# Optimization experiments

Hardware: AMD Instinct MI355X
Metric: run time of the kernel (lower is better)

Reference implementation:

```python
import jax, jax.numpy as jnp
import numpy as np

N, D, E = 100000, 64, 1250000


def setup_inputs() -> dict:
    key = jax.random.key(0)
    k0, k1, k2, k3, k4 = jax.random.split(key, 5)
    return {
        "old_g": jax.random.normal(k0, (N, D), dtype=jnp.float32),        # node DB features
        "W": jax.random.normal(k1, (D, D), dtype=jnp.float32) / np.sqrt(D).astype(np.float32),  # method params
        "edge_weight": jax.random.uniform(k2, (E, 1), dtype=jnp.float32), # per-edge method values
        "history_db": jnp.zeros((N, D), dtype=jnp.float32),               # db_layer.history_db
        "src": jax.random.randint(k3, (E,), 0, N, dtype=jnp.int32),       # gather pattern (sender)
        "dst": jax.random.randint(k4, (E,), 0, N, dtype=jnp.int32),       # scatter index (receiver)
    }


def reference(old_g, W, edge_weight, history_db, src, dst):
    # grab_db_to_method: transform node DB once, then irregular per-edge gather of rows
    h = old_g @ W                                   # [N, D]
    # calc_batch: per-edge method call on gathered sender/receiver features
    msg = jnp.tanh(h[src] + old_g[dst] * edge_weight)  # [E, D]
    # finish_step: scatter-add results back into node-indexed state arrays
    agg = jax.ops.segment_sum(msg, dst, num_segments=old_g.shape[0])  # [N, D]
    nodes_new = agg                   # nodes.at[idx].set(all_results)
    history_new = history_db + agg    # history_db.at[idx].add(all_results)
    return nodes_new, history_new
```

## Files before the change

### kernel.cpp

```cpp
#include <hip/hip_runtime.h>
#include <hip/hip_bf16.h>
#include <hip/hip_fp16.h>


#define D_FEAT 64
#define WQ_SCALE 32767.0f
#define WQ_INV   (1.0f / 32767.0f)
#define BSHIFT 9
#define BN     (1 << BSHIFT)
#define NBUCK_MAX 256
#define BCAP   8192
#define PA_BLOCKS 512
#define PA_CHUNK_MAX 2560

typedef int v4i __attribute__((ext_vector_type(4)));
typedef int v2i __attribute__((ext_vector_type(2)));

#define GR 128
#define GPAD 66

__global__ __launch_bounds__(256) void gemm64_tile_kernel(
    const float* __restrict__ g, const float* __restrict__ W,
    __half* __restrict__ h16, int N, int* __restrict__ bcur) {
    __shared__ float Wl[D_FEAT * D_FEAT];
    __shared__ float Gl[GR][GPAD];

    const int tid = threadIdx.x;

    if (blockIdx.x == 0) bcur[tid] = tid * BCAP;

    {
        const float4* w4 = reinterpret_cast<const float4*>(W);
        float4* wl4 = reinterpret_cast<float4*>(Wl);
        for (int i = tid; i < D_FEAT * D_FEAT / 4; i += 256) wl4[i] = w4[i];
    }

    const int row0  = blockIdx.x * GR;
    const int nrows = min(GR, N - row0);

    for (int i = tid; i < GR * 16; i += 256) {
        const int r  = i >> 4;
        const int c4 = i & 15;
        if (r < nrows) {
            float4 v = reinterpret_cast<const float4*>(
                           g + (size_t)(row0 + r) * D_FEAT)[c4];
            float* dp = &Gl[r][c4 * 4];
            reinterpret_cast<float2*>(dp)[0] = make_float2(v.x, v.y);
            reinterpret_cast<float2*>(dp)[1] = make_float2(v.z, v.w);
        }
    }
    __syncthreads();

    const int cg = tid & 7;
    const int rg = tid >> 3;
    const int c0 = cg * 8;
    const int r0 = rg * 4;

    float acc[4][8];
#pragma unroll
    for (int i = 0; i < 4; ++i)
#pragma unroll
        for (int j = 0; j < 8; ++j) acc[i][j] = 0.0f;

#pragma unroll 4
    for (int k = 0; k < D_FEAT; ++k) {
        const float4 wa = *reinterpret_cast<const float4*>(&Wl[k * D_FEAT + c0]);
        const float4 wb = *reinterpret_cast<const float4*>(&Wl[k * D_FEAT + c0 + 4]);
        float gv[4];
#pragma unroll
        for (int i = 0; i < 4; ++i) gv[i] = Gl[r0 + i][k];
#pragma unroll
        for (int i = 0; i < 4; ++i) {
            acc[i][0] = fmaf(gv[i], wa.x, acc[i][0]);
            acc[i][1] = fmaf(gv[i], wa.y, acc[i][1]);
            acc[i][2] = fmaf(gv[i], wa.z, acc[i][2]);
            acc[i][3] = fmaf(gv[i], wa.w, acc[i][3]);
            acc[i][4] = fmaf(gv[i], wb.x, acc[i][4]);
            acc[i][5] = fmaf(gv[i], wb.y, acc[i][5]);
            acc[i][6] = fmaf(gv[i], wb.z, acc[i][6]);
            acc[i][7] = fmaf(gv[i], wb.w, acc[i][7]);
        }
    }

#pragma unroll
    for (int i = 0; i < 4; ++i) {
        const int r = r0 + i;
        if (r < nrows) {
            __half2 hb[4];
#pragma unroll
            for (int j = 0; j < 4; ++j)
                hb[j] = __floats2half2_rn(acc[i][2 * j], acc[i][2 * j + 1]);
            *reinterpret_cast<uint4*>(h16 + (size_t)(row0 + r) * D_FEAT + c0) =
                *reinterpret_cast<uint4*>(hb);
        }
    }
}

__device__ __forceinline__ unsigned pack_edge(int s, float w) {
    int wq = __float2int_rn(w * WQ_SCALE);
    wq = min(wq, 32767);
    wq = max(wq, 0);
    return (unsigned)s | ((unsigned)wq << 17);
}

__global__ __launch_bounds__(256) void bucketA_kernel(
    const int* __restrict__ src, const int* __restrict__ dst,
    const float* __restrict__ ew, int* __restrict__ bcur,
    int2* __restrict__ staged, int E, int chunk, int nbuck) {
    __shared__ int2 stage[PA_CHUNK_MAX];
    __shared__ int cnt[NBUCK_MAX], startb[NBUCK_MAX], baseb[NBUCK_MAX],
                   cnt2[NBUCK_MAX], sc[NBUCK_MAX];
    const int tid = threadIdx.x;
    const int beg = blockIdx.x * chunk;
    const int end = min(beg + chunk, E);
    const int n = end - beg;
    if (n <= 0) return;

    if (tid < NBUCK_MAX) { cnt[tid] = 0; cnt2[tid] = 0; }
    __syncthreads();

    for (int i = tid; i < n; i += 256)
        atomicAdd(&cnt[dst[beg + i] >> BSHIFT], 1);
    __syncthreads();

    sc[tid] = (tid < nbuck) ? cnt[tid] : 0;
    __syncthreads();
    for (int off = 1; off < NBUCK_MAX; off <<= 1) {
        int x = (tid >= off) ? sc[tid - off] : 0;
        __syncthreads();
        sc[tid] += x;
        __syncthreads();
    }
    if (tid < nbuck) {
        startb[tid] = sc[tid] - cnt[tid];
        if (cnt[tid] > 0) baseb[tid] = atomicAdd(&bcur[tid], cnt[tid]);
    }
    __syncthreads();

    for (int i = tid; i < n; i += 256) {
        const int d = dst[beg + i];
        const int b = d >> BSHIFT;
        const unsigned pl = pack_edge(src[beg + i], ew[beg + i]);
        const int lp = atomicAdd(&cnt2[b], 1);
        stage[startb[b] + lp] = make_int2(d, (int)pl);
    }
    __syncthreads();

    for (int i = tid; i < n; i += 256) {
        const int2 en = stage[i];
        const int b = en.x >> BSHIFT;
        staged[baseb[b] + (i - startb[b])] = en;
    }
}

__global__ __launch_bounds__(256) void bucketB_kernel(
    const int2* __restrict__ staged, const int* __restrict__ bcur,
    int2* __restrict__ nodeinfo, unsigned* __restrict__ srcw,
    int N, int nbuck) {
    __shared__ int cnt[BN];
    __shared__ int cur[BN];
    __shared__ int sc[256];
    const int b = blockIdx.x;
    const int tid = threadIdx.x;
    const int node0 = b << BSHIFT;
    const int beg = b * BCAP;
    const int end = bcur[b];

    cnt[tid] = 0;
    cnt[tid + 256] = 0;
    __syncthreads();

    for (int i = beg + tid; i < end; i += 256) {
        const int2 en = staged[i];
        atomicAdd(&cnt[en.x - node0], 1);
    }
    __syncthreads();

    const int c0 = cnt[2 * tid];
    const int c1 = cnt[2 * tid + 1];
    const int s = c0 + c1;
    sc[tid] = s;
    __syncthreads();
    for (int off = 1; off < 256; off <<= 1) {
        int x = (tid >= off) ? sc[tid - off] : 0;
        __syncthreads();
        sc[tid] += x;
        __syncthreads();
    }
    const int excl = sc[tid] - s + beg;
    {
        const int n0 = node0 + 2 * tid;
        if (n0 < N) {
            nodeinfo[n0] = make_int2(excl, c0);
            cur[2 * tid] = excl;
        }
        if (n0 + 1 < N) {
            nodeinfo[n0 + 1] = make_int2(excl + c0, c1);
            cur[2 * tid + 1] = excl + c0;
        }
    }
    __syncthreads();

    for (int i = beg + tid; i < end; i += 256) {
        const int2 en = staged[i];
        const int pos = atomicAdd(&cur[en.x - node0], 1);
        srcw[pos] = (unsigned)en.y;
    }
}

__device__ __forceinline__ float fast_tanh(float x) {
    float e = __builtin_amdgcn_exp2f(2.885390082f * x);
    float r = __builtin_amdgcn_rcpf(1.0f + e);
    return fmaf(-2.0f, r, 1.0f);
}

__global__ void node_kernel(const __half* __restrict__ h16,
                            const float* __restrict__ g,
                            const float* __restrict__ hist,
                            const int2* __restrict__ nodeinfo,
                            const unsigned* __restrict__ srcw,
                            float* __restrict__ out_nodes,
                            float* __restrict__ out_hist, int N) {
    const int lane = threadIdx.x & 63;
    const int wid  = threadIdx.x >> 6;
    const int wpb  = blockDim.x >> 6;
    const int slot = lane >> 4;
    const int fg   = lane & 15;

    for (int n = blockIdx.x * wpb + wid; n < N; n += gridDim.x * wpb) {
        const int2 info = nodeinfo[n];
        const int beg = info.x;
        const int end = beg + info.y;
        const float4 gd = *reinterpret_cast<const float4*>(
            g + (size_t)n * D_FEAT + fg * 4);
        const float4 hv4 = *reinterpret_cast<const float4*>(
            hist + (size_t)n * D_FEAT + fg * 4);

        float4 acc = make_float4(0.0f, 0.0f, 0.0f, 0.0f);

        for (int base = beg; base < end; base += 64) {
            const int chunk = min(64, end - base);
            const unsigned my_sw = srcw[base + min(lane, chunk - 1)];

            for (int g0 = 0; g0 < chunk; g0 += 8) {
                const int ia = g0 + slot;
                const int ib = ia + 4;
                const unsigned pa = (unsigned)__shfl((int)my_sw, ia, 64);
                const unsigned pb = (unsigned)__shfl((int)my_sw, ib, 64);
                const int   sa = pa & 0x1FFFF;
                const float wa = (float)(pa >> 17) * WQ_INV;
                const int   sb = pb & 0x1FFFF;
                const float wb = (float)(pb >> 17) * WQ_INV;
                const bool va = ia < chunk;
                const bool vb = ib < chunk;
                const uint2 hva = *reinterpret_cast<const uint2*>(
                    h16 + (size_t)sa * D_FEAT + fg * 4);
                const uint2 hvb = *reinterpret_cast<const uint2*>(
                    h16 + (size_t)sb * D_FEAT + fg * 4);

                const float2 a0 = __half22float2(
                    *reinterpret_cast<const __half2*>(&hva.x));
                const float2 a1 = __half22float2(
                    *reinterpret_cast<const __half2*>(&hva.y));
                const float ma = va ? 1.0f : 0.0f;
                acc.x = fmaf(ma, fast_tanh(fmaf(gd.x, wa, a0.x)), acc.x);
                acc.y = fmaf(ma, fast_tanh(fmaf(gd.y, wa, a0.y)), acc.y);
                acc.z = fmaf(ma, fast_tanh(fmaf(gd.z, wa, a1.x)), acc.z);
                acc.w = fmaf(ma, fast_tanh(fmaf(gd.w, wa, a1.y)), acc.w);

                const float2 b0 = __half22float2(
                    *reinterpret_cast<const __half2*>(&hvb.x));
                const float2 b1 = __half22float2(
                    *reinterpret_cast<const __half2*>(&hvb.y));
                const float mb = vb ? 1.0f : 0.0f;
                acc.x = fmaf(mb, fast_tanh(fmaf(gd.x, wb, b0.x)), acc.x);
                acc.y = fmaf(mb, fast_tanh(fmaf(gd.y, wb, b0.y)), acc.y);
                acc.z = fmaf(mb, fast_tanh(fmaf(gd.z, wb, b1.x)), acc.z);
                acc.w = fmaf(mb, fast_tanh(fmaf(gd.w, wb, b1.y)), acc.w);
            }
        }

        acc.x += __shfl_xor(acc.x, 16, 64);
        acc.y += __shfl_xor(acc.y, 16, 64);
        acc.z += __shfl_xor(acc.z, 16, 64);
        acc.w += __shfl_xor(acc.w, 16, 64);
        acc.x += __shfl_xor(acc.x, 32, 64);
        acc.y += __shfl_xor(acc.y, 32, 64);
        acc.z += __shfl_xor(acc.z, 32, 64);
        acc.w += __shfl_xor(acc.w, 32, 64);

        if (lane < 16) {
            reinterpret_cast<float4*>(out_nodes + (size_t)n * D_FEAT)[fg] = acc;
            float4 o;
            o.x = acc.x + hv4.x;
            o.y = acc.y + hv4.y;
            o.z = acc.z + hv4.z;
            o.w = acc.w + hv4.w;
            reinterpret_cast<float4*>(out_hist + (size_t)n * D_FEAT)[fg] = o;
        }
    }
}

extern "C" void kernel_launch(void* const* d_in, const int* in_sizes, int n_in,
                              void* d_out, int out_size, void* d_ws, size_t ws_size,
                              hipStream_t stream) {
    const float* old_g = (const float*)d_in[0];
    const float* W     = (const float*)d_in[1];
    const float* ew    = (const float*)d_in[2];
    const float* hist  = (const float*)d_in[3];
    const int*   src   = (const int*)d_in[4];
    const int*   dst   = (const int*)d_in[5];

    const int N  = in_sizes[0] / D_FEAT;
    const int E  = in_sizes[4];
    const int ND = N * D_FEAT;
    const int nbuck = (N + BN - 1) >> BSHIFT;

    float* out_nodes = (float*)d_out;
    float* out_hist  = (float*)d_out + ND;

    char* ws = (char*)d_ws;
    __half* h16     = (__half*)ws;               ws += (size_t)ND * 2;
    int*  bcur      = (int*)ws;                  ws += 256 * 4;
    int2* nodeinfo  = (int2*)ws;                 ws += (size_t)(N + 2) * 8;
    unsigned* srcw  = (unsigned*)ws;             ws += (size_t)nbuck * BCAP * 4;
    int2* staged    = (int2*)ws;

    {
        int grid = (N + GR - 1) / GR;
        gemm64_tile_kernel<<<grid, 256, 0, stream>>>(old_g, W, h16, N, bcur);
    }

    {
        const int chunk = (E + PA_BLOCKS - 1) / PA_BLOCKS;
        bucketA_kernel<<<PA_BLOCKS, 256, 0, stream>>>(src, dst, ew, bcur,
                                                      staged, E, chunk, nbuck);
    }

    bucketB_kernel<<<nbuck, 256, 0, stream>>>(staged, bcur, nodeinfo,
                                              srcw, N, nbuck);

    {
        const int block = 256, wpb = block / 64;
        int grid = (N + wpb - 1) / wpb;
        if (grid > 8192) grid = 8192;
        node_kernel<<<grid, block, 0, stream>>>(h16, old_g, hist, nodeinfo,
                                                srcw, out_nodes, out_hist, N);
    }
}
```

Before: 103.7 us.

## Merge GEMM and bucket-partition kernels into one launch with block-range dispatch

The node-feature GEMM and the first edge-bucketing pass now run as a single horizontally fused kernel. Low block indices do the GEMM tile and the rest do bucket partitioning, sharing one shared-memory buffer. Bucket cursors are now zero-initialised by a memset and treated as relative offsets, because the GEMM kernel no longer initialises them before bucketing starts. The aim is to remove one kernel launch boundary and let the two independent phases overlap, at the cost of an extra memset and a larger shared-memory footprint per block.

```diff
diff --git a/kernel.cpp b/kernel.cpp
--- a/kernel.cpp
+++ b/kernel.cpp
@@ -13,88 +13,12 @@
 #define PA_BLOCKS 512
 #define PA_CHUNK_MAX 2560
 
+#define GR 128
+#define GPAD 66
+#define SMEM_BYTES 50176
+
 typedef int v4i __attribute__((ext_vector_type(4)));
 typedef int v2i __attribute__((ext_vector_type(2)));
-
-#define GR 128
-#define GPAD 66
-
-__global__ __launch_bounds__(256) void gemm64_tile_kernel(
-    const float* __restrict__ g, const float* __restrict__ W,
-    __half* __restrict__ h16, int N, int* __restrict__ bcur) {
-    __shared__ float Wl[D_FEAT * D_FEAT];
-    __shared__ float Gl[GR][GPAD];
-
-    const int tid = threadIdx.x;
-
-    if (blockIdx.x == 0) bcur[tid] = tid * BCAP;
-
-    {
-        const float4* w4 = reinterpret_cast<const float4*>(W);
-        float4* wl4 = reinterpret_cast<float4*>(Wl);
-        for (int i = tid; i < D_FEAT * D_FEAT / 4; i += 256) wl4[i] = w4[i];
-    }
-
-    const int row0  = blockIdx.x * GR;
-    const int nrows = min(GR, N - row0);
-
-    for (int i = tid; i < GR * 16; i += 256) {
-        const int r  = i >> 4;
-        const int c4 = i & 15;
-        if (r < nrows) {
-            float4 v = reinterpret_cast<const float4*>(
-                           g + (size_t)(row0 + r) * D_FEAT)[c4];
-            float* dp = &Gl[r][c4 * 4];
-            reinterpret_cast<float2*>(dp)[0] = make_float2(v.x, v.y);
-            reinterpret_cast<float2*>(dp)[1] = make_float2(v.z, v.w);
-        }
-    }
-    __syncthreads();
-
-    const int cg = tid & 7;
-    const int rg = tid >> 3;
-    const int c0 = cg * 8;
-    const int r0 = rg * 4;
-
-    float acc[4][8];
-#pragma unroll
-    for (int i = 0; i < 4; ++i)
-#pragma unroll
-        for (int j = 0; j < 8; ++j) acc[i][j] = 0.0f;
-
-#pragma unroll 4
-    for (int k = 0; k < D_FEAT; ++k) {
-        const float4 wa = *reinterpret_cast<const float4*>(&Wl[k * D_FEAT + c0]);
-        const float4 wb = *reinterpret_cast<const float4*>(&Wl[k * D_FEAT + c0 + 4]);
-        float gv[4];
-#pragma unroll
-        for (int i = 0; i < 4; ++i) gv[i] = Gl[r0 + i][k];
-#pragma unroll
-        for (int i = 0; i < 4; ++i) {
-            acc[i][0] = fmaf(gv[i], wa.x, acc[i][0]);
-            acc[i][1] = fmaf(gv[i], wa.y, acc[i][1]);
-            acc[i][2] = fmaf(gv[i], wa.z, acc[i][2]);
-            acc[i][3] = fmaf(gv[i], wa.w, acc[i][3]);
-            acc[i][4] = fmaf(gv[i], wb.x, acc[i][4]);
-            acc[i][5] = fmaf(gv[i], wb.y, acc[i][5]);
-            acc[i][6] = fmaf(gv[i], wb.z, acc[i][6]);
-            acc[i][7] = fmaf(gv[i], wb.w, acc[i][7]);
-        }
-    }
-
-#pragma unroll
-    for (int i = 0; i < 4; ++i) {
-        const int r = r0 + i;
-        if (r < nrows) {
-            __half2 hb[4];
-#pragma unroll
-            for (int j = 0; j < 4; ++j)
-                hb[j] = __floats2half2_rn(acc[i][2 * j], acc[i][2 * j + 1]);
-            *reinterpret_cast<uint4*>(h16 + (size_t)(row0 + r) * D_FEAT + c0) =
-                *reinterpret_cast<uint4*>(hb);
-        }
-    }
-}
 
 __device__ __forceinline__ unsigned pack_edge(int s, float w) {
     int wq = __float2int_rn(w * WQ_SCALE);
@@ -103,53 +27,134 @@
     return (unsigned)s | ((unsigned)wq << 17);
 }
 
-__global__ __launch_bounds__(256) void bucketA_kernel(
+__global__ __launch_bounds__(256) void gemm_bucketA_kernel(
+    const float* __restrict__ g, const float* __restrict__ W,
+    __half* __restrict__ h16, int N,
     const int* __restrict__ src, const int* __restrict__ dst,
     const float* __restrict__ ew, int* __restrict__ bcur,
-    int2* __restrict__ staged, int E, int chunk, int nbuck) {
-    __shared__ int2 stage[PA_CHUNK_MAX];
-    __shared__ int cnt[NBUCK_MAX], startb[NBUCK_MAX], baseb[NBUCK_MAX],
-                   cnt2[NBUCK_MAX], sc[NBUCK_MAX];
+    int2* __restrict__ staged, int E, int chunk, int nbuck, int gemmGrid) {
+    __shared__ __align__(16) char smem[SMEM_BYTES];
     const int tid = threadIdx.x;
-    const int beg = blockIdx.x * chunk;
-    const int end = min(beg + chunk, E);
-    const int n = end - beg;
-    if (n <= 0) return;
-
-    if (tid < NBUCK_MAX) { cnt[tid] = 0; cnt2[tid] = 0; }
-    __syncthreads();
-
-    for (int i = tid; i < n; i += 256)
-        atomicAdd(&cnt[dst[beg + i] >> BSHIFT], 1);
-    __syncthreads();
-
-    sc[tid] = (tid < nbuck) ? cnt[tid] : 0;
-    __syncthreads();
-    for (int off = 1; off < NBUCK_MAX; off <<= 1) {
-        int x = (tid >= off) ? sc[tid - off] : 0;
-        __syncthreads();
-        sc[tid] += x;
-        __syncthreads();
-    }
-    if (tid < nbuck) {
-        startb[tid] = sc[tid] - cnt[tid];
-        if (cnt[tid] > 0) baseb[tid] = atomicAdd(&bcur[tid], cnt[tid]);
-    }
-    __syncthreads();
-
-    for (int i = tid; i < n; i += 256) {
-        const int d = dst[beg + i];
-        const int b = d >> BSHIFT;
-        const unsigned pl = pack_edge(src[beg + i], ew[beg + i]);
-        const int lp = atomicAdd(&cnt2[b], 1);
-        stage[startb[b] + lp] = make_int2(d, (int)pl);
-    }
-    __syncthreads();
-
-    for (int i = tid; i < n; i += 256) {
-        const int2 en = stage[i];
-        const int b = en.x >> BSHIFT;
-        staged[baseb[b] + (i - startb[b])] = en;
+
+    if (blockIdx.x < gemmGrid) {
+        float* Wl = reinterpret_cast<float*>(smem);
+        float (*Gl)[GPAD] = reinterpret_cast<float (*)[GPAD]>(smem + 16384);
+
+        {
+            const float4* w4 = reinterpret_cast<const float4*>(W);
+            float4* wl4 = reinterpret_cast<float4*>(Wl);
+            for (int i = tid; i < D_FEAT * D_FEAT / 4; i += 256) wl4[i] = w4[i];
+        }
+
+        const int row0  = blockIdx.x * GR;
+        const int nrows = min(GR, N - row0);
+
+        for (int i = tid; i < GR * 16; i += 256) {
+            const int r  = i >> 4;
+            const int c4 = i & 15;
+            if (r < nrows) {
+                float4 v = reinterpret_cast<const float4*>(
+                               g + (size_t)(row0 + r) * D_FEAT)[c4];
+                float* dp = &Gl[r][c4 * 4];
+                reinterpret_cast<float2*>(dp)[0] = make_float2(v.x, v.y);
+                reinterpret_cast<float2*>(dp)[1] = make_float2(v.z, v.w);
+            }
+        }
+        __syncthreads();
+
+        const int cg = tid & 7;
+        const int rg = tid >> 3;
+        const int c0 = cg * 8;
+        const int r0 = rg * 4;
+
+        float acc[4][8];
+#pragma unroll
+        for (int i = 0; i < 4; ++i)
+#pragma unroll
+            for (int j = 0; j < 8; ++j) acc[i][j] = 0.0f;
+
+#pragma unroll 4
+        for (int k = 0; k < D_FEAT; ++k) {
+            const float4 wa = *reinterpret_cast<const float4*>(&Wl[k * D_FEAT + c0]);
+            const float4 wb = *reinterpret_cast<const float4*>(&Wl[k * D_FEAT + c0 + 4]);
+            float gv[4];
+#pragma unroll
+            for (int i = 0; i < 4; ++i) gv[i] = Gl[r0 + i][k];
+#pragma unroll
+            for (int i = 0; i < 4; ++i) {
+                acc[i][0] = fmaf(gv[i], wa.x, acc[i][0]);
+                acc[i][1] = fmaf(gv[i], wa.y, acc[i][1]);
+                acc[i][2] = fmaf(gv[i], wa.z, acc[i][2]);
+                acc[i][3] = fmaf(gv[i], wa.w, acc[i][3]);
+                acc[i][4] = fmaf(gv[i], wb.x, acc[i][4]);
+                acc[i][5] = fmaf(gv[i], wb.y, acc[i][5]);
+                acc[i][6] = fmaf(gv[i], wb.z, acc[i][6]);
+                acc[i][7] = fmaf(gv[i], wb.w, acc[i][7]);
+            }
+        }
+
+#pragma unroll
+        for (int i = 0; i < 4; ++i) {
+            const int r = r0 + i;
+            if (r < nrows) {
+                __half2 hb[4];
+#pragma unroll
+                for (int j = 0; j < 4; ++j)
+                    hb[j] = __floats2half2_rn(acc[i][2 * j], acc[i][2 * j + 1]);
+                *reinterpret_cast<uint4*>(h16 + (size_t)(row0 + r) * D_FEAT + c0) =
+                    *reinterpret_cast<uint4*>(hb);
+            }
+        }
+    } else {
+        int2* stage  = reinterpret_cast<int2*>(smem);
+        int* cnt     = reinterpret_cast<int*>(smem + 20480);
+        int* startb  = reinterpret_cast<int*>(smem + 20480 + 1024);
+        int* baseb   = reinterpret_cast<int*>(smem + 20480 + 2048);
+        int* cnt2    = reinterpret_cast<int*>(smem + 20480 + 3072);
+        int* sc      = reinterpret_cast<int*>(smem + 20480 + 4096);
+
+        const int ab = blockIdx.x - gemmGrid;
+        const int beg = ab * chunk;
+        const int end = min(beg + chunk, E);
+        const int n = end - beg;
+        if (n <= 0) return;
+
+        cnt[tid] = 0;
+        cnt2[tid] = 0;
+        __syncthreads();
+
+        for (int i = tid; i < n; i += 256)
+            atomicAdd(&cnt[dst[beg + i] >> BSHIFT], 1);
+        __syncthreads();
+
+        sc[tid] = (tid < nbuck) ? cnt[tid] : 0;
+        __syncthreads();
+        for (int off = 1; off < NBUCK_MAX; off <<= 1) {
+            int x = (tid >= off) ? sc[tid - off] : 0;
+            __syncthreads();
+            sc[tid] += x;
+            __syncthreads();
+        }
+        if (tid < nbuck) {
+            startb[tid] = sc[tid] - cnt[tid];
+            if (cnt[tid] > 0) baseb[tid] = atomicAdd(&bcur[tid], cnt[tid]);
+        }
+        __syncthreads();
+
+        for (int i = tid; i < n; i += 256) {
+            const int d = dst[beg + i];
+            const int b = d >> BSHIFT;
+            const unsigned pl = pack_edge(src[beg + i], ew[beg + i]);
+            const int lp = atomicAdd(&cnt2[b], 1);
+            stage[startb[b] + lp] = make_int2(d, (int)pl);
+        }
+        __syncthreads();
+
+        for (int i = tid; i < n; i += 256) {
+            const int2 en = stage[i];
+            const int b = en.x >> BSHIFT;
+            staged[(size_t)b * BCAP + baseb[b] + (i - startb[b])] = en;
+        }
     }
 }
 
@@ -164,7 +169,7 @@
     const int tid = threadIdx.x;
     const int node0 = b << BSHIFT;
     const int beg = b * BCAP;
-    const int end = bcur[b];
+    const int end = beg + bcur[b];
 
     cnt[tid] = 0;
     cnt[tid + 256] = 0;
@@ -326,15 +331,14 @@
     unsigned* srcw  = (unsigned*)ws;             ws += (size_t)nbuck * BCAP * 4;
     int2* staged    = (int2*)ws;
 
+    hipMemsetAsync(bcur, 0, 256 * sizeof(int), stream);
+
     {
-        int grid = (N + GR - 1) / GR;
-        gemm64_tile_kernel<<<grid, 256, 0, stream>>>(old_g, W, h16, N, bcur);
-    }
-
-    {
+        const int gemmGrid = (N + GR - 1) / GR;
         const int chunk = (E + PA_BLOCKS - 1) / PA_BLOCKS;
-        bucketA_kernel<<<PA_BLOCKS, 256, 0, stream>>>(src, dst, ew, bcur,
-                                                      staged, E, chunk, nbuck);
+        gemm_bucketA_kernel<<<gemmGrid + PA_BLOCKS, 256, 0, stream>>>(
+            old_g, W, h16, N, src, dst, ew, bcur, staged, E, chunk, nbuck,
+            gemmGrid);
     }
 
     bucketB_kernel<<<nbuck, 256, 0, stream>>>(staged, bcur, nodeinfo,
```

Result: faster. 99.40 us, median of 2 (-4.1%).
